# Kernel tuning notes

Hardware: AMD Instinct MI355X
Metric: run time of the kernel (lower is better)

## Reference

```python
import jax, jax.numpy as jnp
import numpy as np

D_EMB = 1024
N_HEADS = 16
HEAD_DIM = D_EMB // N_HEADS


def _xavier(key, out_f, in_f):
    limit = jnp.sqrt(6.0 / (in_f + out_f))
    return jax.random.uniform(key, (out_f, in_f), jnp.float32, -limit, limit)


def setup_inputs() -> dict:
    key = jax.random.key(0)
    k_x, k_qkv, k_out = jax.random.split(key, 3)
    x = jax.random.normal(k_x, (4, 2048, D_EMB), jnp.float32)
    # torch nn.Linear weights: [out_features, in_features], xavier_uniform; biases zero
    w_qkv = _xavier(k_qkv, 3 * D_EMB, D_EMB)
    b_qkv = jnp.zeros((3 * D_EMB,), jnp.float32)
    w_out = _xavier(k_out, D_EMB, D_EMB)
    b_out = jnp.zeros((D_EMB,), jnp.float32)
    return {"x": x, "w_qkv": w_qkv, "b_qkv": b_qkv, "w_out": w_out, "b_out": b_out}


def reference(x, w_qkv, b_qkv, w_out, b_out):
    B, S, D = x.shape
    # QKV projection: y = x @ W^T + b -> [B, S, 3D]
    qkv = jnp.einsum('bsd,ed->bse', x, w_qkv) + b_qkv
    # view(B, S, H, 3*head_dim) then split into q, k, v (matches torch chunk on last dim)
    qkv = qkv.reshape(B, S, N_HEADS, 3 * HEAD_DIM)
    q, k, v = jnp.split(qkv, 3, axis=-1)  # each [B, S, H, head_dim]
    scale = 1.0 / jnp.sqrt(jnp.float32(HEAD_DIM))
    scores = jnp.einsum('bshd,bthd->bhst', q, k) * scale  # [B, H, S, S]
    probs = jax.nn.softmax(scores, axis=-1)
    out = jnp.einsum('bhst,bthd->bshd', probs, v).reshape(B, S, D)
    return jnp.einsum('bsd,ed->bse', out, w_out) + b_out
```

## Files before the change

kernel.cpp:

```cpp
#include <hip/hip_runtime.h>

typedef __bf16 bf16_t;
typedef __bf16 bf16x8 __attribute__((ext_vector_type(8)));
typedef __bf16 bf16x4 __attribute__((ext_vector_type(4)));
typedef float f32x4 __attribute__((ext_vector_type(4)));

#define S_LEN 2048
#define D_EMB 1024
#define NH 16

#define MFMA16(a, b, c) __builtin_amdgcn_mfma_f32_16x16x32_bf16((a), (b), (c), 0, 0, 0)

__device__ __forceinline__ void gld16(void* lds, const void* g) {
  __builtin_amdgcn_global_load_lds(
      (__attribute__((address_space(1))) void*)(void*)(g),
      (__attribute__((address_space(3))) void*)(lds), 16, 0, 0);
}

__device__ __forceinline__ float exp2_hw(float x) {
  float r;
  asm("v_exp_f32 %0, %1" : "=v"(r) : "v"(x));
  return r;
}

__global__ __launch_bounds__(256) void cvt_bf16(const float* __restrict__ in,
                                                bf16_t* __restrict__ out, int n4) {
  int i = blockIdx.x * 256 + threadIdx.x;
  if (i >= n4) return;
  float4 v = ((const float4*)in)[i];
  bf16x4 o;
  o[0] = (bf16_t)v.x; o[1] = (bf16_t)v.y; o[2] = (bf16_t)v.z; o[3] = (bf16_t)v.w;
  ((bf16x4*)out)[i] = o;
}

template <int EPI>
__global__ __launch_bounds__(256) void gemm_bt(
    const bf16_t* __restrict__ A, const bf16_t* __restrict__ W,
    const float* __restrict__ bias, float* __restrict__ outF,
    bf16_t* __restrict__ outQ, int M, int N, int K) {
  __shared__ __attribute__((aligned(16))) bf16_t As[128 * 64];
  __shared__ __attribute__((aligned(16))) bf16_t Ws[128 * 64];
  const int tid = threadIdx.x;
  const int lane = tid & 63;
  const int wid = tid >> 6;
  const int l15 = lane & 15, lg = lane >> 4;
  int lin = blockIdx.x + gridDim.x * blockIdx.y;
  const int nwg = gridDim.x * gridDim.y;
  lin = (lin & 7) * (nwg >> 3) + (lin >> 3);
  const int tm = (lin / gridDim.x) * 128, tn = (lin % gridDim.x) * 128;
  const int wm = (wid >> 1) * 64, wn = (wid & 1) * 64;
  f32x4 acc[4][4] = {};
  const int q0 = tid * 16;

  for (int k0 = 0; k0 < K; k0 += 64) {
#pragma unroll
    for (int i = 0; i < 4; ++i) {
      int q = q0 + i * 4096;
      int row = q >> 7;
      int scb = (q & 127) ^ ((row & 7) << 4);
      gld16((char*)As + (q & ~1023),
            (const char*)A + ((size_t)(tm + row) * K + k0) * 2 + scb);
      gld16((char*)Ws + (q & ~1023),
            (const char*)W + ((size_t)(tn + row) * K + k0) * 2 + scb);
    }
    __syncthreads();
#pragma unroll
    for (int kk = 0; kk < 2; ++kk) {
      const int cb = kk * 64 + lg * 16;
      bf16x8 af[4], bfr[4];
#pragma unroll
      for (int mi = 0; mi < 4; ++mi) {
        int row = wm + mi * 16 + l15;
        af[mi] = *(const bf16x8*)((const char*)As + row * 128 + (cb ^ ((row & 7) << 4)));
      }
#pragma unroll
      for (int ni = 0; ni < 4; ++ni) {
        int row = wn + ni * 16 + l15;
        bfr[ni] = *(const bf16x8*)((const char*)Ws + row * 128 + (cb ^ ((row & 7) << 4)));
      }
#pragma unroll
      for (int mi = 0; mi < 4; ++mi)
#pragma unroll
        for (int ni = 0; ni < 4; ++ni)
          acc[mi][ni] = MFMA16(af[mi], bfr[ni], acc[mi][ni]);
    }
    __syncthreads();
  }

  if (EPI == 0) {
#pragma unroll
    for (int mi = 0; mi < 4; ++mi)
#pragma unroll
      for (int ni = 0; ni < 4; ++ni) {
        int colg = tn + wn + ni * 16 + l15;
        float bv = bias[colg];
#pragma unroll
        for (int j = 0; j < 4; ++j) {
          int rowg = tm + wm + mi * 16 + lg * 4 + j;
          outF[(size_t)rowg * N + colg] = acc[mi][ni][j] + bv;
        }
      }
  } else {
#pragma unroll
    for (int mi = 0; mi < 4; ++mi)
#pragma unroll
      for (int ni = 0; ni < 4; ++ni) {
        int e = tn + wn + ni * 16 + l15;
        float bv = bias[e];
        int h = e / 192;
        int r = e - h * 192;
        int t = r >> 6, c = r & 63;
#pragma unroll
        for (int j = 0; j < 4; ++j) {
          int m = tm + wm + mi * 16 + lg * 4 + j;
          int b = m >> 11, s = m & 2047;
          float v = acc[mi][ni][j] + bv;
          if (t == 0) v *= 0.18033688011112042f;
          size_t base = ((size_t)(b * NH + h) * 3 + t) * (size_t)(S_LEN * 64);
          size_t idx;
          if (t == 2) {
            int rs = s & 31;
            int rp = (((rs >> 2) & 3) << 3) | ((rs >> 4) << 2) | (rs & 3);
            idx = base + (size_t)c * S_LEN + (size_t)((s & ~31) | rp);
          } else {
            idx = base + (size_t)s * 64 + c;
          }
          outQ[idx] = (bf16_t)v;
        }
      }
  }
}

__global__ __launch_bounds__(256) void attn_fwd(const bf16_t* __restrict__ qkvb,
                                                bf16_t* __restrict__ attnb) {
  __shared__ __attribute__((aligned(16))) bf16_t Ks[3][64 * 64];
  __shared__ __attribute__((aligned(16))) bf16_t Vs[3][64 * 64];
  const int tid = threadIdx.x, lane = tid & 63, wid = tid >> 6;
  const int l15 = lane & 15, lg = lane >> 4;
  int lin = blockIdx.x + (blockIdx.y << 4);
  lin = (lin & 7) * 128 + (lin >> 3);
  const int qt = lin & 15;
  const int bh = lin >> 4;
  const int b = bh >> 4, h = bh & 15;
  const char* Qg = (const char*)qkvb + (size_t)bh * 3 * (S_LEN * 64) * 2;
  const char* Kg = Qg + (size_t)S_LEN * 64 * 2;
  const char* Vtg = Kg + (size_t)S_LEN * 64 * 2;
  const int q0 = tid * 16;

  bf16x8 qf[2][2];
#pragma unroll
  for (int mi = 0; mi < 2; ++mi) {
    const char* qr = Qg + (size_t)(qt * 128 + wid * 32 + mi * 16 + l15) * 128;
#pragma unroll
    for (int kb = 0; kb < 2; ++kb)
      qf[mi][kb] = *(const bf16x8*)(qr + kb * 64 + lg * 16);
  }

  auto stage = [&](int t) {
#pragma unroll
    for (int i = 0; i < 2; ++i) {
      int q = q0 + i * 4096;
      int row = q >> 7;
      int scb = (q & 127) ^ ((row & 7) << 4);
      gld16((char*)Ks[t % 3] + (q & ~1023),
            Kg + (size_t)(t * 64 + row) * 128 + scb);
      gld16((char*)Vs[t % 3] + (q & ~1023),
            Vtg + (size_t)row * (S_LEN * 2) + t * 128 + scb);
    }
  };
  stage(0);
  stage(1);

  float lsum[2] = {0.f, 0.f};
  f32x4 o[2][4] = {};
  const int swk = (l15 & 7) << 4;

  for (int kt = 0; kt < 32; ++kt) {
    if (kt < 31) {
      asm volatile("s_waitcnt vmcnt(4)" ::: "memory");
    } else {
      asm volatile("s_waitcnt vmcnt(0)" ::: "memory");
    }
    __builtin_amdgcn_s_barrier();
    asm volatile("" ::: "memory");
    if (kt + 2 < 32) stage(kt + 2);

    const bf16_t* Kc = Ks[kt % 3];
    const bf16_t* Vc = Vs[kt % 3];

    f32x4 stv[2][4];
#pragma unroll
    for (int nk = 0; nk < 4; ++nk) {
      const char* kr = (const char*)Kc + (nk * 16 + l15) * 128;
      bf16x8 kf0 = *(const bf16x8*)(kr + ((lg * 16) ^ swk));
      bf16x8 kf1 = *(const bf16x8*)(kr + ((64 + lg * 16) ^ swk));
#pragma unroll
      for (int mi = 0; mi < 2; ++mi) {
        f32x4 z = {};
        z = MFMA16(kf0, qf[mi][0], z);
        stv[mi][nk] = MFMA16(kf1, qf[mi][1], z);
      }
    }

#pragma unroll
    for (int mi = 0; mi < 2; ++mi)
#pragma unroll
      for (int nk = 0; nk < 4; ++nk)
#pragma unroll
        for (int j = 0; j < 4; ++j) {
          float p = exp2_hw(stv[mi][nk][j]);
          stv[mi][nk][j] = p;
          lsum[mi] += p;
        }

#pragma unroll
    for (int kp = 0; kp < 2; ++kp) {
      bf16x8 pf[2];
#pragma unroll
      for (int mi = 0; mi < 2; ++mi)
#pragma unroll
        for (int j = 0; j < 4; ++j) {
          pf[mi][j] = (bf16_t)stv[mi][2 * kp][j];
          pf[mi][4 + j] = (bf16_t)stv[mi][2 * kp + 1][j];
        }
#pragma unroll
      for (int ndv = 0; ndv < 4; ++ndv) {
        const char* vr = (const char*)Vc + (ndv * 16 + l15) * 128;
        bf16x8 vf = *(const bf16x8*)(vr + ((kp * 64 + 16 * lg) ^ swk));
        o[0][ndv] = MFMA16(pf[0], vf, o[0][ndv]);
        o[1][ndv] = MFMA16(pf[1], vf, o[1][ndv]);
      }
    }
  }

#pragma unroll
  for (int mi = 0; mi < 2; ++mi) {
    lsum[mi] += __shfl_xor(lsum[mi], 16);
    lsum[mi] += __shfl_xor(lsum[mi], 32);
  }
  float inv[2][4];
#pragma unroll
  for (int mi = 0; mi < 2; ++mi)
#pragma unroll
    for (int j = 0; j < 4; ++j)
      inv[mi][j] = 1.0f / __shfl(lsum[mi], (lane & 48) | (lg * 4 + j));

#pragma unroll
  for (int mi = 0; mi < 2; ++mi)
#pragma unroll
    for (int j = 0; j < 4; ++j) {
      int srow = qt * 128 + wid * 32 + mi * 16 + lg * 4 + j;
      bf16_t* dst = attnb + ((size_t)b * S_LEN + srow) * D_EMB + h * 64;
#pragma unroll
      for (int ndv = 0; ndv < 4; ++ndv)
        dst[ndv * 16 + l15] = (bf16_t)(o[mi][ndv][j] * inv[mi][j]);
    }
}

extern "C" void kernel_launch(void* const* d_in, const int* in_sizes, int n_in,
                              void* d_out, int out_size, void* d_ws, size_t ws_size,
                              hipStream_t stream) {
  const float* x = (const float*)d_in[0];
  const float* w_qkv = (const float*)d_in[1];
  const float* b_qkv = (const float*)d_in[2];
  const float* w_out = (const float*)d_in[3];
  const float* b_out = (const float*)d_in[4];
  float* out = (float*)d_out;

  bf16_t* xb = (bf16_t*)d_ws;
  bf16_t* wqkvb = xb + 8388608;
  bf16_t* woutb = wqkvb + 3145728;
  bf16_t* qkvb = woutb + 1048576;
  bf16_t* attnb = qkvb + 25165824;

  cvt_bf16<<<8192, 256, 0, stream>>>(x, xb, 2097152);
  cvt_bf16<<<3072, 256, 0, stream>>>(w_qkv, wqkvb, 786432);
  cvt_bf16<<<1024, 256, 0, stream>>>(w_out, woutb, 262144);

  gemm_bt<1><<<dim3(24, 64), 256, 0, stream>>>(xb, wqkvb, b_qkv, nullptr, qkvb,
                                               8192, 3072, 1024);
  attn_fwd<<<dim3(16, 64), 256, 0, stream>>>(qkvb, attnb);
  gemm_bt<0><<<dim3(8, 64), 256, 0, stream>>>(attnb, woutb, b_out, out, nullptr,
                                              8192, 1024, 1024);
}
```

Measured before the change: 212.2 us.

## Software-pipeline attention loop: overlap next QK with current PV, deepen LDS ring

Restructures the attention inner loop so the QK^T MFMAs for tile kt+1 are issued together with the PV MFMAs for tile kt, while the exp/convert softmax work for tile kt+1 runs afterwards. The goal is to hide the transcendental and convert latency behind matrix-core work. The K/V LDS ring grows from 3 to 4 buffers with a prefetch distance of 3, and s_setprio raises wave priority around the MFMA section. The cost is more LDS per block, which may reduce occupancy, and more live registers for the carried pf and stv fragments.

After: 205.2 us. 3.3% less time.

```diff
diff --git a/kernel.cpp b/kernel.cpp
--- a/kernel.cpp
+++ b/kernel.cpp
@@ -133,8 +133,8 @@
 
 __global__ __launch_bounds__(256) void attn_fwd(const bf16_t* __restrict__ qkvb,
                                                 bf16_t* __restrict__ attnb) {
-  __shared__ __attribute__((aligned(16))) bf16_t Ks[3][64 * 64];
-  __shared__ __attribute__((aligned(16))) bf16_t Vs[3][64 * 64];
+  __shared__ __attribute__((aligned(16))) bf16_t Ks[4][64 * 64];
+  __shared__ __attribute__((aligned(16))) bf16_t Vs[4][64 * 64];
   const int tid = threadIdx.x, lane = tid & 63, wid = tid >> 6;
   const int l15 = lane & 15, lg = lane >> 4;
   int lin = blockIdx.x + (blockIdx.y << 4);
@@ -162,33 +162,19 @@
       int q = q0 + i * 4096;
       int row = q >> 7;
       int scb = (q & 127) ^ ((row & 7) << 4);
-      gld16((char*)Ks[t % 3] + (q & ~1023),
+      gld16((char*)Ks[t & 3] + (q & ~1023),
             Kg + (size_t)(t * 64 + row) * 128 + scb);
-      gld16((char*)Vs[t % 3] + (q & ~1023),
+      gld16((char*)Vs[t & 3] + (q & ~1023),
             Vtg + (size_t)row * (S_LEN * 2) + t * 128 + scb);
     }
   };
-  stage(0);
-  stage(1);
 
   float lsum[2] = {0.f, 0.f};
   f32x4 o[2][4] = {};
+  bf16x8 pf[2][2];
   const int swk = (l15 & 7) << 4;
 
-  for (int kt = 0; kt < 32; ++kt) {
-    if (kt < 31) {
-      asm volatile("s_waitcnt vmcnt(4)" ::: "memory");
-    } else {
-      asm volatile("s_waitcnt vmcnt(0)" ::: "memory");
-    }
-    __builtin_amdgcn_s_barrier();
-    asm volatile("" ::: "memory");
-    if (kt + 2 < 32) stage(kt + 2);
-
-    const bf16_t* Kc = Ks[kt % 3];
-    const bf16_t* Vc = Vs[kt % 3];
-
-    f32x4 stv[2][4];
+  auto QK = [&](const bf16_t* Kc, f32x4(&stv)[2][4]) {
 #pragma unroll
     for (int nk = 0; nk < 4; ++nk) {
       const char* kr = (const char*)Kc + (nk * 16 + l15) * 128;
@@ -201,7 +187,8 @@
         stv[mi][nk] = MFMA16(kf1, qf[mi][1], z);
       }
     }
-
+  };
+  auto SM = [&](f32x4(&stv)[2][4]) {
 #pragma unroll
     for (int mi = 0; mi < 2; ++mi)
 #pragma unroll
@@ -212,26 +199,64 @@
           stv[mi][nk][j] = p;
           lsum[mi] += p;
         }
-
-#pragma unroll
-    for (int kp = 0; kp < 2; ++kp) {
-      bf16x8 pf[2];
+#pragma unroll
+    for (int kp = 0; kp < 2; ++kp)
 #pragma unroll
       for (int mi = 0; mi < 2; ++mi)
 #pragma unroll
         for (int j = 0; j < 4; ++j) {
-          pf[mi][j] = (bf16_t)stv[mi][2 * kp][j];
-          pf[mi][4 + j] = (bf16_t)stv[mi][2 * kp + 1][j];
+          pf[kp][mi][j] = (bf16_t)stv[mi][2 * kp][j];
+          pf[kp][mi][4 + j] = (bf16_t)stv[mi][2 * kp + 1][j];
         }
+  };
+  auto PV = [&](const bf16_t* Vc) {
+#pragma unroll
+    for (int kp = 0; kp < 2; ++kp)
 #pragma unroll
       for (int ndv = 0; ndv < 4; ++ndv) {
         const char* vr = (const char*)Vc + (ndv * 16 + l15) * 128;
         bf16x8 vf = *(const bf16x8*)(vr + ((kp * 64 + 16 * lg) ^ swk));
-        o[0][ndv] = MFMA16(pf[0], vf, o[0][ndv]);
-        o[1][ndv] = MFMA16(pf[1], vf, o[1][ndv]);
-      }
-    }
-  }
+        o[0][ndv] = MFMA16(pf[kp][0], vf, o[0][ndv]);
+        o[1][ndv] = MFMA16(pf[kp][1], vf, o[1][ndv]);
+      }
+  };
+
+  stage(0); stage(1); stage(2);
+  asm volatile("s_waitcnt vmcnt(8)" ::: "memory");
+  __builtin_amdgcn_s_barrier();
+  asm volatile("" ::: "memory");
+  {
+    f32x4 stv[2][4];
+    __builtin_amdgcn_s_setprio(1);
+    QK(Ks[0], stv);
+    __builtin_amdgcn_s_setprio(0);
+    SM(stv);
+  }
+
+  for (int kt = 0; kt < 30; ++kt) {
+    asm volatile("s_waitcnt vmcnt(4)" ::: "memory");
+    __builtin_amdgcn_s_barrier();
+    asm volatile("" ::: "memory");
+    if (kt + 3 < 32) stage(kt + 3);
+    f32x4 stv[2][4];
+    __builtin_amdgcn_s_setprio(1);
+    QK(Ks[(kt + 1) & 3], stv);
+    PV(Vs[kt & 3]);
+    __builtin_amdgcn_s_setprio(0);
+    SM(stv);
+  }
+  asm volatile("s_waitcnt vmcnt(0)" ::: "memory");
+  __builtin_amdgcn_s_barrier();
+  asm volatile("" ::: "memory");
+  {
+    f32x4 stv[2][4];
+    __builtin_amdgcn_s_setprio(1);
+    QK(Ks[31 & 3], stv);
+    PV(Vs[30 & 3]);
+    __builtin_amdgcn_s_setprio(0);
+    SM(stv);
+  }
+  PV(Vs[31 & 3]);
 
 #pragma unroll
   for (int mi = 0; mi < 2; ++mi) {
```
